# Kernel tuning notes

Hardware: AMD Instinct MI355X
Metric: run time of the kernel (lower is better)

Reference implementation:

```python
import jax, jax.numpy as jnp
import numpy as np

N, E, D, L = 50000, 400000, 128, 5
EPS = 1e-5  # BatchNorm1d default eps


def setup_inputs() -> dict:
    key = jax.random.key(0)
    ks = jax.random.split(key, 9)
    x = jax.random.normal(ks[0], (N, D), jnp.float32)
    edge_index = jax.random.randint(ks[1], (2, E), 0, N)
    edge_attr = jax.random.normal(ks[2], (E, 4), jnp.float32)
    # per-layer params (stacked over L layers)
    W1 = jax.random.normal(ks[3], (L, 3, D), jnp.float32) * (6.0 / (3 + D)) ** 0.5
    W2 = jax.random.normal(ks[4], (L, 1, D), jnp.float32) * (6.0 / (1 + D)) ** 0.5
    Wm = jax.random.normal(ks[5], (L, D, 2 * D), jnp.float32) * (6.0 / (3 * D)) ** 0.5
    bm = jnp.zeros((L, D), jnp.float32)
    gamma = jnp.ones((L, D), jnp.float32)
    beta = jnp.zeros((L, D), jnp.float32)
    return dict(x=x, edge_index=edge_index, edge_attr=edge_attr,
                W1=W1, W2=W2, Wm=Wm, bm=bm, gamma=gamma, beta=beta)


def reference(x, edge_index, edge_attr, W1, W2, Wm, bm, gamma, beta):
    row, col = edge_index[0], edge_index[1]
    # symmetric GCN norm: deg computed by scattering ones at col
    deg = jax.ops.segment_sum(jnp.ones((E,), x.dtype), col, num_segments=N)
    deg_safe = jnp.where(deg > 0, deg, 1.0)
    dinv = jnp.where(deg > 0, deg_safe ** -0.5, 0.0)  # [N]
    norm = dinv[row] * dinv[col]                      # [E]

    h = x
    for l in range(L):
        # edge feature projection ('2-3d'): first 3 cols @ W1 + last col @ W2
        edge_fea = edge_attr[:, :3] @ W1[l] + edge_attr[:, 3:] @ W2[l]  # [E, D]
        # message: norm * (x_j + edge_fea), gather at source (row)
        msg = norm[:, None] * (h[row] + edge_fea)                       # [E, D]
        # aggregate: scatter-add at target (col)
        agg = jax.ops.segment_sum(msg, col, num_segments=N)             # [N, D]
        # mlp(concat([x, out])) with ReLU
        h2 = jax.nn.relu(jnp.concatenate([h, agg], axis=1) @ Wm[l].T + bm[l])
        # BatchNorm1d (training mode: batch stats, biased variance)
        mean = h2.mean(axis=0)
        var = jnp.mean((h2 - mean) ** 2, axis=0)
        h = gamma[l] * (h2 - mean) * jax.lax.rsqrt(var + EPS) + beta[l]
        if l < L - 1:
            h = jax.nn.relu(h)
        # dropout p=0 -> identity
    return h
```

## Files before the change

### kernel.cpp

```cpp
#include <hip/hip_runtime.h>

#define D 128
#define EPSBN 1e-5f
#define PB 800
#define GROWS 64
#define GBK 64

typedef __attribute__((ext_vector_type(8))) short bf16x8;
typedef __attribute__((ext_vector_type(4))) float f32x4;

static __device__ __forceinline__ unsigned short f2b(float f) {
    unsigned u = __float_as_uint(f);
    unsigned r = u + 0x7FFF + ((u >> 16) & 1);
    return (unsigned short)(r >> 16);
}
static __device__ __forceinline__ float b2f_lo(unsigned p) { return __uint_as_float(p << 16); }
static __device__ __forceinline__ float b2f_hi(unsigned p) { return __uint_as_float(p & 0xFFFF0000u); }

static __device__ __forceinline__ unsigned short f2h(float f) {
    _Float16 h = (_Float16)f;
    unsigned short u;
    __builtin_memcpy(&u, &h, 2);
    return u;
}
static __device__ __forceinline__ float h2f(unsigned short u) {
    _Float16 h;
    __builtin_memcpy(&h, &u, 2);
    return (float)h;
}
static __device__ __forceinline__ float h2f_lo(unsigned p) { return h2f((unsigned short)(p & 0xFFFF)); }
static __device__ __forceinline__ float h2f_hi(unsigned p) { return h2f((unsigned short)(p >> 16)); }


__global__ void k_deg(const int* __restrict__ ei, int E, int* __restrict__ deg,
                      int* __restrict__ pos) {
    int e = blockIdx.x * 256 + threadIdx.x;
    if (e < E) pos[e] = atomicAdd(&deg[ei[E + e]], 1);
}

__global__ void k_bsum(const int* __restrict__ deg, int* __restrict__ bsum, int N) {
    __shared__ int sm[256];
    int t = threadIdx.x, v = blockIdx.x * 256 + t;
    sm[t] = (v < N) ? deg[v] : 0;
    __syncthreads();
    for (int off = 128; off > 0; off >>= 1) {
        if (t < off) sm[t] += sm[t + off];
        __syncthreads();
    }
    if (t == 0) bsum[blockIdx.x] = sm[0];
}

__global__ void k_bscan(const int* __restrict__ bsum, int* __restrict__ boff,
                        int* __restrict__ row_ptr, int NB, int N, int E) {
    __shared__ int sm[256];
    int t = threadIdx.x;
    int v = (t < NB) ? bsum[t] : 0;
    sm[t] = v;
    __syncthreads();
    for (int off = 1; off < 256; off <<= 1) {
        int x = (t >= off) ? sm[t - off] : 0;
        __syncthreads();
        sm[t] += x;
        __syncthreads();
    }
    if (t < NB) boff[t] = sm[t] - v;
    if (t == 0) row_ptr[N] = E;
}

__global__ void k_scatter(const int* __restrict__ deg, const int* __restrict__ boff,
                          int* __restrict__ row_ptr, int N) {
    __shared__ int sm[256];
    int t = threadIdx.x, v = blockIdx.x * 256 + t;
    int val = (v < N) ? deg[v] : 0;
    sm[t] = val;
    __syncthreads();
    for (int off = 1; off < 256; off <<= 1) {
        int x = (t >= off) ? sm[t - off] : 0;
        __syncthreads();
        sm[t] += x;
        __syncthreads();
    }
    if (v < N) row_ptr[v] = boff[blockIdx.x] + sm[t] - val;
}

__global__ void k_place(const int* __restrict__ ei, const int* __restrict__ row_ptr,
                        const int* __restrict__ pos, int2* __restrict__ csr, int E) {
    int e = blockIdx.x * 256 + threadIdx.x;
    if (e >= E) return;
    int c = ei[E + e];
    csr[row_ptr[c] + pos[e]] = make_int2(ei[e], e);
}

__global__ void k_cvals(const int* __restrict__ row_ptr, int2* __restrict__ csr,
                        const int* __restrict__ deg, const float* __restrict__ attr,
                        float4* __restrict__ cvals, int N) {
    int v = blockIdx.x * 256 + threadIdx.x;
    if (v >= N) return;
    int dgv = deg[v];
    float dv = (dgv > 0) ? rsqrtf((float)dgv) : 0.f;
    int jb = row_ptr[v], je = row_ptr[v + 1];
    float4 acc = make_float4(0.f, 0.f, 0.f, 0.f);
    for (int j = jb; j < je; ++j) {
        int2 e = csr[j];
        int dgs = deg[e.x];
        float ds = (dgs > 0) ? rsqrtf((float)dgs) : 0.f;
        float nm = ds * dv;
        float4 a = *(const float4*)(attr + (size_t)e.y * 4);
        acc.x += nm * a.x; acc.y += nm * a.y;
        acc.z += nm * a.z; acc.w += nm * a.w;
        csr[j] = make_int2(e.x, __float_as_int(nm));
    }
    cvals[v] = acc;
}

__global__ void k_cvt(const float* __restrict__ in, unsigned short* __restrict__ outp, int n4) {
    int i = blockIdx.x * 256 + threadIdx.x;
    if (i >= n4) return;
    float4 v = *(const float4*)(in + (size_t)i * 4);
    ushort4 p;
    p.x = f2b(v.x); p.y = f2b(v.y); p.z = f2b(v.z); p.w = f2b(v.w);
    *(ushort4*)(outp + (size_t)i * 4) = p;
}


__global__ __launch_bounds__(256) void k_spmm(
        const unsigned short* __restrict__ hb, const int* __restrict__ row_ptr,
        const int2* __restrict__ csr, const float4* __restrict__ cvals,
        const float* __restrict__ W1l, const float* __restrict__ W2l,
        const float* __restrict__ scsh, int apply,
        unsigned short* __restrict__ aggb, int N) {
    int lane = threadIdx.x & 63;
    int v = blockIdx.x * 4 + (threadIdx.x >> 6);
    if (v >= N) return;
    int qw = lane >> 4;
    int l4 = lane & 15;
    int d0 = l4 * 8;
    int jb = row_ptr[v], je = row_ptr[v + 1];

    float a[8];
#pragma unroll
    for (int i = 0; i < 8; ++i) a[i] = 0.f;

    if (apply) {
        float sc[8], sh[8];
#pragma unroll
        for (int i = 0; i < 8; i += 4) {
            float4 s = *(const float4*)(scsh + d0 + i);
            float4 t = *(const float4*)(scsh + D + d0 + i);
            sc[i] = s.x; sc[i + 1] = s.y; sc[i + 2] = s.z; sc[i + 3] = s.w;
            sh[i] = t.x; sh[i + 1] = t.y; sh[i + 2] = t.z; sh[i + 3] = t.w;
        }
        for (int j0 = jb; j0 < je; j0 += 8) {
            int ja = j0 + qw, jc = j0 + 4 + qw;
            bool oa = (ja < je), oc = (jc < je);
            int2 ea = csr[oa ? ja : jb];
            int2 ec = csr[oc ? jc : jb];
            float na = oa ? __int_as_float(ea.y) : 0.f;
            float nc = oc ? __int_as_float(ec.y) : 0.f;
            uint4 pa = *(const uint4*)(hb + (size_t)ea.x * D + d0);
            uint4 pc = *(const uint4*)(hb + (size_t)ec.x * D + d0);
            float xa[8] = {h2f_lo(pa.x), h2f_hi(pa.x), h2f_lo(pa.y), h2f_hi(pa.y),
                           h2f_lo(pa.z), h2f_hi(pa.z), h2f_lo(pa.w), h2f_hi(pa.w)};
            float xc[8] = {h2f_lo(pc.x), h2f_hi(pc.x), h2f_lo(pc.y), h2f_hi(pc.y),
                           h2f_lo(pc.z), h2f_hi(pc.z), h2f_lo(pc.w), h2f_hi(pc.w)};
#pragma unroll
            for (int i = 0; i < 8; ++i) {
                a[i] += na * fmaxf(sc[i] * xa[i] + sh[i], 0.f);
                a[i] += nc * fmaxf(sc[i] * xc[i] + sh[i], 0.f);
            }
        }
    } else {
        for (int j0 = jb; j0 < je; j0 += 8) {
            int ja = j0 + qw, jc = j0 + 4 + qw;
            bool oa = (ja < je), oc = (jc < je);
            int2 ea = csr[oa ? ja : jb];
            int2 ec = csr[oc ? jc : jb];
            float na = oa ? __int_as_float(ea.y) : 0.f;
            float nc = oc ? __int_as_float(ec.y) : 0.f;
            uint4 pa = *(const uint4*)(hb + (size_t)ea.x * D + d0);
            uint4 pc = *(const uint4*)(hb + (size_t)ec.x * D + d0);
            a[0] += na * b2f_lo(pa.x) + nc * b2f_lo(pc.x);
            a[1] += na * b2f_hi(pa.x) + nc * b2f_hi(pc.x);
            a[2] += na * b2f_lo(pa.y) + nc * b2f_lo(pc.y);
            a[3] += na * b2f_hi(pa.y) + nc * b2f_hi(pc.y);
            a[4] += na * b2f_lo(pa.z) + nc * b2f_lo(pc.z);
            a[5] += na * b2f_hi(pa.z) + nc * b2f_hi(pc.z);
            a[6] += na * b2f_lo(pa.w) + nc * b2f_lo(pc.w);
            a[7] += na * b2f_hi(pa.w) + nc * b2f_hi(pc.w);
        }
    }
#pragma unroll
    for (int i = 0; i < 8; ++i) {
        a[i] += __shfl_xor(a[i], 16);
        a[i] += __shfl_xor(a[i], 32);
    }
    if (qw == 0) {
        float4 c = cvals[v];
        float4 wa0 = *(const float4*)(W1l + d0);
        float4 wa1 = *(const float4*)(W1l + d0 + 4);
        float4 wb0 = *(const float4*)(W1l + D + d0);
        float4 wb1 = *(const float4*)(W1l + D + d0 + 4);
        float4 wc0 = *(const float4*)(W1l + 2 * D + d0);
        float4 wc1 = *(const float4*)(W1l + 2 * D + d0 + 4);
        float4 wd0 = *(const float4*)(W2l + d0);
        float4 wd1 = *(const float4*)(W2l + d0 + 4);
        a[0] += c.x * wa0.x + c.y * wb0.x + c.z * wc0.x + c.w * wd0.x;
        a[1] += c.x * wa0.y + c.y * wb0.y + c.z * wc0.y + c.w * wd0.y;
        a[2] += c.x * wa0.z + c.y * wb0.z + c.z * wc0.z + c.w * wd0.z;
        a[3] += c.x * wa0.w + c.y * wb0.w + c.z * wc0.w + c.w * wd0.w;
        a[4] += c.x * wa1.x + c.y * wb1.x + c.z * wc1.x + c.w * wd1.x;
        a[5] += c.x * wa1.y + c.y * wb1.y + c.z * wc1.y + c.w * wd1.y;
        a[6] += c.x * wa1.z + c.y * wb1.z + c.z * wc1.z + c.w * wd1.z;
        a[7] += c.x * wa1.w + c.y * wb1.w + c.z * wc1.w + c.w * wd1.w;
        uint4 o;
        o.x = ((unsigned)f2b(a[1]) << 16) | (unsigned)f2b(a[0]);
        o.y = ((unsigned)f2b(a[3]) << 16) | (unsigned)f2b(a[2]);
        o.z = ((unsigned)f2b(a[5]) << 16) | (unsigned)f2b(a[4]);
        o.w = ((unsigned)f2b(a[7]) << 16) | (unsigned)f2b(a[6]);
        *(uint4*)(aggb + (size_t)v * D + d0) = o;
    }
}

__global__ __launch_bounds__(256) void k_gemm(
        const unsigned short* __restrict__ hsrc, const unsigned short* __restrict__ aggb,
        const unsigned short* __restrict__ Wmb, const float* __restrict__ bml,
        const float* __restrict__ scsh, int apply,
        unsigned short* __restrict__ h2h, float* __restrict__ pbuf, int N) {
    __shared__ unsigned short As[GROWS][GBK + 8];
    __shared__ unsigned short Bs[D][GBK + 8];
    __shared__ float sred[2][4][D];
    int tid = threadIdx.x;
    int lane = tid & 63, wave = tid >> 6;
    int n0 = blockIdx.x * GROWS;
    int l15 = lane & 15, q = lane >> 4;
    f32x4 acc[8];
#pragma unroll
    for (int t = 0; t < 8; ++t) acc[t] = (f32x4){0.f, 0.f, 0.f, 0.f};

    for (int kc = 0; kc < 4; ++kc) {
        const unsigned short* src = (kc < 2) ? hsrc : aggb;
        bool aff = (kc < 2) && apply;
        int k0 = (kc & 1) * GBK;
#pragma unroll
        for (int i = 0; i < 2; ++i) {
            int idx = tid + i * 256;
            int r = idx >> 3, seg = idx & 7;
            uint4 val = make_uint4(0u, 0u, 0u, 0u);
            if (n0 + r < N) val = *(const uint4*)(src + (size_t)(n0 + r) * D + k0 + seg * 8);
            if (aff) {
                int db = k0 + seg * 8;
                float4 s0 = *(const float4*)(scsh + db);
                float4 s1 = *(const float4*)(scsh + db + 4);
                float4 t0 = *(const float4*)(scsh + D + db);
                float4 t1 = *(const float4*)(scsh + D + db + 4);
                float e0 = fmaxf(s0.x * h2f_lo(val.x) + t0.x, 0.f);
                float e1 = fmaxf(s0.y * h2f_hi(val.x) + t0.y, 0.f);
                float e2 = fmaxf(s0.z * h2f_lo(val.y) + t0.z, 0.f);
                float e3 = fmaxf(s0.w * h2f_hi(val.y) + t0.w, 0.f);
                float e4 = fmaxf(s1.x * h2f_lo(val.z) + t1.x, 0.f);
                float e5 = fmaxf(s1.y * h2f_hi(val.z) + t1.y, 0.f);
                float e6 = fmaxf(s1.z * h2f_lo(val.w) + t1.z, 0.f);
                float e7 = fmaxf(s1.w * h2f_hi(val.w) + t1.w, 0.f);
                val.x = ((unsigned)f2b(e1) << 16) | (unsigned)f2b(e0);
                val.y = ((unsigned)f2b(e3) << 16) | (unsigned)f2b(e2);
                val.z = ((unsigned)f2b(e5) << 16) | (unsigned)f2b(e4);
                val.w = ((unsigned)f2b(e7) << 16) | (unsigned)f2b(e6);
            }
            *(uint4*)&As[r][seg * 8] = val;
        }
#pragma unroll
        for (int i = 0; i < 4; ++i) {
            int idx = tid + i * 256;
            int n = idx >> 3, seg = idx & 7;
            *(uint4*)&Bs[n][seg * 8] =
                *(const uint4*)(Wmb + (size_t)n * 256 + kc * GBK + seg * 8);
        }
        __syncthreads();
#pragma unroll
        for (int s = 0; s < 2; ++s) {
            bf16x8 a = *(const bf16x8*)&As[wave * 16 + l15][s * 32 + q * 8];
#pragma unroll
            for (int t = 0; t < 8; ++t) {
                bf16x8 b = *(const bf16x8*)&Bs[t * 16 + l15][s * 32 + q * 8];
                acc[t] = __builtin_amdgcn_mfma_f32_16x16x32_bf16(a, b, acc[t], 0, 0, 0);
            }
        }
        __syncthreads();
    }
    bool full = (n0 + GROWS <= N);
    float ps[8], pq[8];
#pragma unroll
    for (int t = 0; t < 8; ++t) {
        int n = t * 16 + l15;
        float bias = bml[n];
        float s = 0.f, qs = 0.f;
#pragma unroll
        for (int r = 0; r < 4; ++r) {
            int m = n0 + wave * 16 + q * 4 + r;
            float v = fmaxf(acc[t][r] + bias, 0.f);
            if (full || m < N) {
                h2h[(size_t)m * D + n] = f2h(v);
                s += v; qs += v * v;
            }
        }
        ps[t] = s; pq[t] = qs;
    }
#pragma unroll
    for (int t = 0; t < 8; ++t) {
        ps[t] += __shfl_xor(ps[t], 16); ps[t] += __shfl_xor(ps[t], 32);
        pq[t] += __shfl_xor(pq[t], 16); pq[t] += __shfl_xor(pq[t], 32);
    }
    if (q == 0) {
#pragma unroll
        for (int t = 0; t < 8; ++t) {
            sred[0][wave][t * 16 + l15] = ps[t];
            sred[1][wave][t * 16 + l15] = pq[t];
        }
    }
    __syncthreads();
    if (tid < D) {
        float s = sred[0][0][tid] + sred[0][1][tid] + sred[0][2][tid] + sred[0][3][tid];
        pbuf[(size_t)tid * PB + blockIdx.x] = s;
    } else {
        int n = tid - D;
        float qv = sred[1][0][n] + sred[1][1][n] + sred[1][2][n] + sred[1][3][n];
        pbuf[(size_t)(n + D) * PB + blockIdx.x] = qv;
    }
}

__global__ __launch_bounds__(128) void k_reduce(
        const float* __restrict__ pbuf, const float* __restrict__ gam,
        const float* __restrict__ bet, float* __restrict__ scsh, int nb, int N) {
    int n = blockIdx.x;
    int t = threadIdx.x;
    float s = 0.f, qv = 0.f;
    for (int b = t; b < nb; b += 128) {
        s  += pbuf[(size_t)n * PB + b];
        qv += pbuf[(size_t)(n + D) * PB + b];
    }
#pragma unroll
    for (int off = 32; off > 0; off >>= 1) {
        s += __shfl_down(s, off);
        qv += __shfl_down(qv, off);
    }
    __shared__ float aux[4];
    if ((t & 63) == 0) { aux[t >> 6] = s; aux[2 + (t >> 6)] = qv; }
    __syncthreads();
    if (t == 0) {
        float S = aux[0] + aux[1], Q = aux[2] + aux[3];
        float mean = S / (float)N;
        float var = fmaxf(Q / (float)N - mean * mean, 0.f);
        float sc = gam[n] * rsqrtf(var + EPSBN);
        scsh[n] = sc;
        scsh[D + n] = bet[n] - mean * sc;
    }
}

__global__ void k_norm_last(const unsigned short* __restrict__ h2h,
                            const float* __restrict__ scsh,
                            float* __restrict__ out_f, int total4) {
    int i = blockIdx.x * 256 + threadIdx.x;
    if (i >= total4) return;
    int base = i * 4;
    int d = base & (D - 1);
    uint2 p = *(const uint2*)(h2h + base);
    float4 o;
    o.x = scsh[d + 0] * h2f_lo(p.x) + scsh[D + d + 0];
    o.y = scsh[d + 1] * h2f_hi(p.x) + scsh[D + d + 1];
    o.z = scsh[d + 2] * h2f_lo(p.y) + scsh[D + d + 2];
    o.w = scsh[d + 3] * h2f_hi(p.y) + scsh[D + d + 3];
    *(float4*)(out_f + base) = o;
}


extern "C" void kernel_launch(void* const* d_in, const int* in_sizes, int n_in,
                              void* d_out, int out_size, void* d_ws, size_t ws_size,
                              hipStream_t stream) {
    const float* x    = (const float*)d_in[0];
    const int*   ei   = (const int*)d_in[1];
    const float* attr = (const float*)d_in[2];
    const float* W1   = (const float*)d_in[3];
    const float* W2   = (const float*)d_in[4];
    const float* Wm   = (const float*)d_in[5];
    const float* bm   = (const float*)d_in[6];
    const float* gam  = (const float*)d_in[7];
    const float* bet  = (const float*)d_in[8];
    float* out = (float*)d_out;

    const int N = in_sizes[0] / D;
    const int E = in_sizes[1] / 2;
    const int L = in_sizes[3] / (3 * D);
    const int NB = (N + 255) / 256;

    size_t off = 0;
    auto carve = [&](size_t bytes) {
        void* p = (char*)d_ws + off;
        off += (bytes + 255) & ~(size_t)255;
        return p;
    };
    int*            deg     = (int*)carve((size_t)N * 4);
    int*            row_ptr = (int*)carve((size_t)(N + 1) * 4);
    int*            pos     = (int*)carve((size_t)E * 4);
    int*            bsum    = (int*)carve((size_t)NB * 4);
    int*            boff    = (int*)carve((size_t)NB * 4);
    int2*           csr     = (int2*)carve((size_t)(E + 8) * 8);
    float4*         cvals   = (float4*)carve((size_t)N * 16);
    unsigned short* xb      = (unsigned short*)carve((size_t)N * D * 2);
    unsigned short* h2h     = (unsigned short*)carve((size_t)N * D * 2);
    unsigned short* aggb    = (unsigned short*)carve((size_t)N * D * 2);
    unsigned short* Wmb     = (unsigned short*)carve((size_t)L * D * 256 * 2);
    float*          pbuf    = (float*)carve((size_t)2 * D * PB * 4);
    float*          scsh    = (float*)carve((size_t)2 * D * 4);
    (void)ws_size;

    hipMemsetAsync(deg, 0, (size_t)N * 4, stream);

    const int eb = (E + 255) / 256;
    k_deg<<<eb, 256, 0, stream>>>(ei, E, deg, pos);
    k_bsum<<<NB, 256, 0, stream>>>(deg, bsum, N);
    k_bscan<<<1, 256, 0, stream>>>(bsum, boff, row_ptr, NB, N, E);
    k_scatter<<<NB, 256, 0, stream>>>(deg, boff, row_ptr, N);
    k_place<<<eb, 256, 0, stream>>>(ei, row_ptr, pos, csr, E);
    k_cvals<<<NB, 256, 0, stream>>>(row_ptr, csr, deg, attr, cvals, N);

    const int xq = N * D / 4;
    k_cvt<<<(xq + 255) / 256, 256, 0, stream>>>(x, xb, xq);
    const int wq = L * D * 256 / 4;
    k_cvt<<<(wq + 255) / 256, 256, 0, stream>>>(Wm, Wmb, wq);

    const int total4 = N * D / 4;
    const int nt = (N + GROWS - 1) / GROWS;
    const int spmmb = (N + 3) / 4;

    for (int l = 0; l < L; ++l) {
        const unsigned short* in = (l == 0) ? xb : h2h;
        const int apply = (l > 0) ? 1 : 0;
        const float* W1l = W1 + (size_t)l * 3 * D;
        const float* W2l = W2 + (size_t)l * D;
        const unsigned short* Wml = Wmb + (size_t)l * D * 256;
        const float* bml = bm + (size_t)l * D;

        k_spmm<<<spmmb, 256, 0, stream>>>(in, row_ptr, csr, cvals, W1l, W2l,
                                          scsh, apply, aggb, N);
        k_gemm<<<nt, 256, 0, stream>>>(in, aggb, Wml, bml, scsh, apply,
                                       h2h, pbuf, N);
        k_reduce<<<D, 128, 0, stream>>>(pbuf, gam + (size_t)l * D,
                                        bet + (size_t)l * D, scsh, nt, N);
    }
    k_norm_last<<<(total4 + 255) / 256, 256, 0, stream>>>(h2h, scsh, out, total4);
}
```

Measured before the change: 420.5 us.

## Pack two nodes per wave in SpMM and two row tiles per GEMM block

```diff
diff --git a/kernel.cpp b/kernel.cpp
--- a/kernel.cpp
+++ b/kernel.cpp
@@ -2,7 +2,7 @@
 
 #define D 128
 #define EPSBN 1e-5f
-#define PB 800
+#define PB 400
 #define GROWS 64
 #define GBK 64
 
@@ -130,9 +130,11 @@
         const float* __restrict__ scsh, int apply,
         unsigned short* __restrict__ aggb, int N) {
     int lane = threadIdx.x & 63;
-    int v = blockIdx.x * 4 + (threadIdx.x >> 6);
+    int wave = threadIdx.x >> 6;
+    int nh = lane >> 5;
+    int v = blockIdx.x * 8 + wave * 2 + nh;
     if (v >= N) return;
-    int qw = lane >> 4;
+    int qw = (lane >> 4) & 1;
     int l4 = lane & 15;
     int d0 = l4 * 8;
     int jb = row_ptr[v], je = row_ptr[v + 1];
@@ -150,8 +152,8 @@
             sc[i] = s.x; sc[i + 1] = s.y; sc[i + 2] = s.z; sc[i + 3] = s.w;
             sh[i] = t.x; sh[i + 1] = t.y; sh[i + 2] = t.z; sh[i + 3] = t.w;
         }
-        for (int j0 = jb; j0 < je; j0 += 8) {
-            int ja = j0 + qw, jc = j0 + 4 + qw;
+        for (int j0 = jb; j0 < je; j0 += 4) {
+            int ja = j0 + qw, jc = j0 + 2 + qw;
             bool oa = (ja < je), oc = (jc < je);
             int2 ea = csr[oa ? ja : jb];
             int2 ec = csr[oc ? jc : jb];
@@ -170,8 +172,8 @@
             }
         }
     } else {
-        for (int j0 = jb; j0 < je; j0 += 8) {
-            int ja = j0 + qw, jc = j0 + 4 + qw;
+        for (int j0 = jb; j0 < je; j0 += 4) {
+            int ja = j0 + qw, jc = j0 + 2 + qw;
             bool oa = (ja < je), oc = (jc < je);
             int2 ea = csr[oa ? ja : jb];
             int2 ec = csr[oc ? jc : jb];
@@ -190,10 +192,8 @@
         }
     }
 #pragma unroll
-    for (int i = 0; i < 8; ++i) {
-        a[i] += __shfl_xor(a[i], 16);
-        a[i] += __shfl_xor(a[i], 32);
-    }
+    for (int i = 0; i < 8; ++i) a[i] += __shfl_xor(a[i], 16);
+
     if (qw == 0) {
         float4 c = cvals[v];
         float4 wa0 = *(const float4*)(W1l + d0);
@@ -226,47 +226,53 @@
         const unsigned short* __restrict__ Wmb, const float* __restrict__ bml,
         const float* __restrict__ scsh, int apply,
         unsigned short* __restrict__ h2h, float* __restrict__ pbuf, int N) {
-    __shared__ unsigned short As[GROWS][GBK + 8];
+    __shared__ unsigned short As[2][GROWS][GBK + 8];
     __shared__ unsigned short Bs[D][GBK + 8];
     __shared__ float sred[2][4][D];
     int tid = threadIdx.x;
     int lane = tid & 63, wave = tid >> 6;
-    int n0 = blockIdx.x * GROWS;
+    int n0a = blockIdx.x * (2 * GROWS);
     int l15 = lane & 15, q = lane >> 4;
-    f32x4 acc[8];
-#pragma unroll
-    for (int t = 0; t < 8; ++t) acc[t] = (f32x4){0.f, 0.f, 0.f, 0.f};
+    f32x4 acc[2][8];
+#pragma unroll
+    for (int t2 = 0; t2 < 2; ++t2)
+#pragma unroll
+        for (int t = 0; t < 8; ++t) acc[t2][t] = (f32x4){0.f, 0.f, 0.f, 0.f};
 
     for (int kc = 0; kc < 4; ++kc) {
         const unsigned short* src = (kc < 2) ? hsrc : aggb;
         bool aff = (kc < 2) && apply;
         int k0 = (kc & 1) * GBK;
 #pragma unroll
-        for (int i = 0; i < 2; ++i) {
-            int idx = tid + i * 256;
-            int r = idx >> 3, seg = idx & 7;
-            uint4 val = make_uint4(0u, 0u, 0u, 0u);
-            if (n0 + r < N) val = *(const uint4*)(src + (size_t)(n0 + r) * D + k0 + seg * 8);
-            if (aff) {
-                int db = k0 + seg * 8;
-                float4 s0 = *(const float4*)(scsh + db);
-                float4 s1 = *(const float4*)(scsh + db + 4);
-                float4 t0 = *(const float4*)(scsh + D + db);
-                float4 t1 = *(const float4*)(scsh + D + db + 4);
-                float e0 = fmaxf(s0.x * h2f_lo(val.x) + t0.x, 0.f);
-                float e1 = fmaxf(s0.y * h2f_hi(val.x) + t0.y, 0.f);
-                float e2 = fmaxf(s0.z * h2f_lo(val.y) + t0.z, 0.f);
-                float e3 = fmaxf(s0.w * h2f_hi(val.y) + t0.w, 0.f);
-                float e4 = fmaxf(s1.x * h2f_lo(val.z) + t1.x, 0.f);
-                float e5 = fmaxf(s1.y * h2f_hi(val.z) + t1.y, 0.f);
-                float e6 = fmaxf(s1.z * h2f_lo(val.w) + t1.z, 0.f);
-                float e7 = fmaxf(s1.w * h2f_hi(val.w) + t1.w, 0.f);
-                val.x = ((unsigned)f2b(e1) << 16) | (unsigned)f2b(e0);
-                val.y = ((unsigned)f2b(e3) << 16) | (unsigned)f2b(e2);
-                val.z = ((unsigned)f2b(e5) << 16) | (unsigned)f2b(e4);
-                val.w = ((unsigned)f2b(e7) << 16) | (unsigned)f2b(e6);
+        for (int t2 = 0; t2 < 2; ++t2) {
+#pragma unroll
+            for (int i = 0; i < 2; ++i) {
+                int idx = tid + i * 256;
+                int r = idx >> 3, seg = idx & 7;
+                int m = n0a + t2 * GROWS + r;
+                uint4 val = make_uint4(0u, 0u, 0u, 0u);
+                if (m < N) val = *(const uint4*)(src + (size_t)m * D + k0 + seg * 8);
+                if (aff) {
+                    int db = k0 + seg * 8;
+                    float4 s0 = *(const float4*)(scsh + db);
+                    float4 s1 = *(const float4*)(scsh + db + 4);
+                    float4 t0 = *(const float4*)(scsh + D + db);
+                    float4 t1 = *(const float4*)(scsh + D + db + 4);
+                    float e0 = fmaxf(s0.x * h2f_lo(val.x) + t0.x, 0.f);
+                    float e1 = fmaxf(s0.y * h2f_hi(val.x) + t0.y, 0.f);
+                    float e2 = fmaxf(s0.z * h2f_lo(val.y) + t0.z, 0.f);
+                    float e3 = fmaxf(s0.w * h2f_hi(val.y) + t0.w, 0.f);
+                    float e4 = fmaxf(s1.x * h2f_lo(val.z) + t1.x, 0.f);
+                    float e5 = fmaxf(s1.y * h2f_hi(val.z) + t1.y, 0.f);
+                    float e6 = fmaxf(s1.z * h2f_lo(val.w) + t1.z, 0.f);
+                    float e7 = fmaxf(s1.w * h2f_hi(val.w) + t1.w, 0.f);
+                    val.x = ((unsigned)f2b(e1) << 16) | (unsigned)f2b(e0);
+                    val.y = ((unsigned)f2b(e3) << 16) | (unsigned)f2b(e2);
+                    val.z = ((unsigned)f2b(e5) << 16) | (unsigned)f2b(e4);
+                    val.w = ((unsigned)f2b(e7) << 16) | (unsigned)f2b(e6);
+                }
+                *(uint4*)&As[t2][r][seg * 8] = val;
             }
-            *(uint4*)&As[r][seg * 8] = val;
         }
 #pragma unroll
         for (int i = 0; i < 4; ++i) {
@@ -278,32 +284,38 @@
         __syncthreads();
 #pragma unroll
         for (int s = 0; s < 2; ++s) {
-            bf16x8 a = *(const bf16x8*)&As[wave * 16 + l15][s * 32 + q * 8];
+            bf16x8 a0 = *(const bf16x8*)&As[0][wave * 16 + l15][s * 32 + q * 8];
+            bf16x8 a1 = *(const bf16x8*)&As[1][wave * 16 + l15][s * 32 + q * 8];
 #pragma unroll
             for (int t = 0; t < 8; ++t) {
                 bf16x8 b = *(const bf16x8*)&Bs[t * 16 + l15][s * 32 + q * 8];
-                acc[t] = __builtin_amdgcn_mfma_f32_16x16x32_bf16(a, b, acc[t], 0, 0, 0);
+                acc[0][t] = __builtin_amdgcn_mfma_f32_16x16x32_bf16(a0, b, acc[0][t], 0, 0, 0);
+                acc[1][t] = __builtin_amdgcn_mfma_f32_16x16x32_bf16(a1, b, acc[1][t], 0, 0, 0);
             }
         }
         __syncthreads();
     }
-    bool full = (n0 + GROWS <= N);
     float ps[8], pq[8];
 #pragma unroll
-    for (int t = 0; t < 8; ++t) {
-        int n = t * 16 + l15;
-        float bias = bml[n];
-        float s = 0.f, qs = 0.f;
-#pragma unroll
-        for (int r = 0; r < 4; ++r) {
-            int m = n0 + wave * 16 + q * 4 + r;
-            float v = fmaxf(acc[t][r] + bias, 0.f);
-            if (full || m < N) {
-                h2h[(size_t)m * D + n] = f2h(v);
-                s += v; qs += v * v;
+    for (int t = 0; t < 8; ++t) { ps[t] = 0.f; pq[t] = 0.f; }
+#pragma unroll
+    for (int t2 = 0; t2 < 2; ++t2) {
+        int n0 = n0a + t2 * GROWS;
+        bool full = (n0 + GROWS <= N);
+#pragma unroll
+        for (int t = 0; t < 8; ++t) {
+            int n = t * 16 + l15;
+            float bias = bml[n];
+#pragma unroll
+            for (int r = 0; r < 4; ++r) {
+                int m = n0 + wave * 16 + q * 4 + r;
+                float v = fmaxf(acc[t2][t][r] + bias, 0.f);
+                if (full || m < N) {
+                    h2h[(size_t)m * D + n] = f2h(v);
+                    ps[t] += v; pq[t] += v * v;
+                }
             }
         }
-        ps[t] = s; pq[t] = qs;
     }
 #pragma unroll
     for (int t = 0; t < 8; ++t) {
@@ -429,8 +441,8 @@
     k_cvt<<<(wq + 255) / 256, 256, 0, stream>>>(Wm, Wmb, wq);
 
     const int total4 = N * D / 4;
-    const int nt = (N + GROWS - 1) / GROWS;
-    const int spmmb = (N + 3) / 4;
+    const int gemmb = (N + 2 * GROWS - 1) / (2 * GROWS);
+    const int spmmb = (N + 7) / 8;
 
     for (int l = 0; l < L; ++l) {
         const unsigned short* in = (l == 0) ? xb : h2h;
@@ -442,10 +454,10 @@
 
         k_spmm<<<spmmb, 256, 0, stream>>>(in, row_ptr, csr, cvals, W1l, W2l,
                                           scsh, apply, aggb, N);
-        k_gemm<<<nt, 256, 0, stream>>>(in, aggb, Wml, bml, scsh, apply,
-                                       h2h, pbuf, N);
+        k_gemm<<<gemmb, 256, 0, stream>>>(in, aggb, Wml, bml, scsh, apply,
+                                          h2h, pbuf, N);
         k_reduce<<<D, 128, 0, stream>>>(pbuf, gam + (size_t)l * D,
-                                        bet + (size_t)l * D, scsh, nt, N);
+                                        bet + (size_t)l * D, scsh, gemmb, N);
     }
     k_norm_last<<<(total4 + 255) / 256, 256, 0, stream>>>(h2h, scsh, out, total4);
 }
```

Result: faster. 388.9 us (-7.5%).
